# Performance work log

Hardware: AMD Instinct MI355X
Metric: run time of the kernel (lower is better)

## Reference

```python
import jax, jax.numpy as jnp
import numpy as np


def setup_inputs() -> dict:
    key = jax.random.key(0)
    k1, k2, k3, k4 = jax.random.split(key, 4)
    B, NITER, NSIZE, DIM = 4096, 8, 32, 64
    return {
        "self_vectors": jax.random.normal(k1, (B, NITER, DIM), dtype=jnp.float32),
        "neighbor_vectors": jax.random.normal(k2, (B, NITER * NSIZE, DIM), dtype=jnp.float32),
        "neighbor_relations": jax.random.normal(k3, (B, NITER * NSIZE, DIM), dtype=jnp.float32),
        "user_embeddings": jax.random.normal(k4, (B, DIM), dtype=jnp.float32),
        "neighbor_size": NSIZE,
    }


def reference(self_vectors, neighbor_vectors, neighbor_relations, user_embeddings, neighbor_size):
    B, neighbor_iter, dim = self_vectors.shape
    # reshape flat neighbor axis -> (B, neighbor_iter, neighbor_size, dim)
    nv = neighbor_vectors.reshape(B, neighbor_iter, neighbor_size, dim)
    nr = neighbor_relations.reshape(B, neighbor_iter, neighbor_size, dim)
    ue = user_embeddings.reshape(B, 1, 1, dim)
    # user-relation attention score per neighbor: mean over dim
    scores = jnp.mean(ue * nr, axis=-1)                       # [B, niter, nsize]
    weights = jax.nn.softmax(scores, axis=-1)[..., None]      # [B, niter, nsize, 1]
    # softmax-weighted neighbors, then mean over neighbor axis
    neighbors_aggregated = jnp.mean(weights * nv, axis=2)     # [B, niter, dim]
    return jax.nn.relu(neighbors_aggregated)
```

## Files before the change

### kernel.cpp

```cpp
#include <hip/hip_runtime.h>


constexpr int DIM = 64;
constexpr int NSIZE = 32;

__global__ __launch_bounds__(256) void Aggregator_kernel(
    const float* __restrict__ nv,
    const float* __restrict__ nr,
    const float* __restrict__ ue,
    float* __restrict__ out,
    int niter, int ntasks) {
  int wave = (int)((blockIdx.x * blockDim.x + threadIdx.x) >> 6);
  if (wave >= ntasks) return;
  int lane = (int)(threadIdx.x & 63);
  int b = wave / niter;

  const float* nr_base = nr + (size_t)wave * (NSIZE * DIM);
  const float* nv_base = nv + (size_t)wave * (NSIZE * DIM);
  const float* ue_base = ue + (size_t)b * DIM;

  int h = lane >> 5;
  int s = lane & 31;

  const float4* nr4 = (const float4*)(nr_base + s * DIM + h * 32);
  const float4* ue4 = (const float4*)(ue_base + h * 32);
  float p = 0.f;
#pragma unroll
  for (int j = 0; j < 8; ++j) {
    float4 a = nr4[j];
    float4 u = ue4[j];
    p = fmaf(a.x, u.x, p);
    p = fmaf(a.y, u.y, p);
    p = fmaf(a.z, u.z, p);
    p = fmaf(a.w, u.w, p);
  }
  p += __shfl_xor(p, 32);
  float sc = p * (1.0f / DIM);

  float m = sc;
#pragma unroll
  for (int k = 1; k < 32; k <<= 1) m = fmaxf(m, __shfl_xor(m, k));
  float e = __expf(sc - m);
  float sum = e;
#pragma unroll
  for (int k = 1; k < 32; k <<= 1) sum += __shfl_xor(sum, k);
  float w = e / (sum * (float)NSIZE);

  float acc = 0.f;
#pragma unroll
  for (int si = 0; si < NSIZE; ++si) {
    float ws = __int_as_float(__builtin_amdgcn_readlane(__float_as_int(w), si));
    acc = fmaf(ws, nv_base[si * DIM + lane], acc);
  }
  out[(size_t)wave * DIM + lane] = fmaxf(acc, 0.f);
}

extern "C" void kernel_launch(void* const* d_in, const int* in_sizes, int n_in,
                              void* d_out, int out_size, void* d_ws, size_t ws_size,
                              hipStream_t stream) {
  const float* nv = (const float*)d_in[1];
  const float* nr = (const float*)d_in[2];
  const float* ue = (const float*)d_in[3];
  float* out = (float*)d_out;

  int ntasks = in_sizes[0] / DIM;
  int niter  = in_sizes[0] / in_sizes[3];
  int blocks = (ntasks + 3) / 4;
  Aggregator_kernel<<<blocks, 256, 0, stream>>>(nv, nr, ue, out, niter, ntasks);
}
```

Measured before the change: 513.5 us.

## Remap lanes for fully coalesced float4 loads and issue all loads upfront

Each wave now loads its neighbor relations and neighbor vectors as contiguous float4 chunks. Lane q=lane&15 covers a 4-wide slice of dim, and each lane handles 8 neighbors. All 16 float4 loads are issued before any compute, to raise memory-level parallelism and cut the strided and scalar load patterns of the old code. The dot products, softmax and weighted sum are rebuilt around this layout using 16-lane shuffle reductions and cross-group shuffles. This costs more registers and extra shuffles, and only 16 lanes write the output as float4.

After: 514.4 us. Within noise of the previous version (+0.2%).

```diff
diff --git a/kernel.cpp b/kernel.cpp
--- a/kernel.cpp
+++ b/kernel.cpp
@@ -14,45 +14,68 @@
   if (wave >= ntasks) return;
   int lane = (int)(threadIdx.x & 63);
   int b = wave / niter;
+  int q = lane & 15;
 
-  const float* nr_base = nr + (size_t)wave * (NSIZE * DIM);
-  const float* nv_base = nv + (size_t)wave * (NSIZE * DIM);
-  const float* ue_base = ue + (size_t)b * DIM;
+  const float4* nr4 = (const float4*)(nr + (size_t)wave * (NSIZE * DIM));
+  const float4* nv4 = (const float4*)(nv + (size_t)wave * (NSIZE * DIM));
 
-  int h = lane >> 5;
-  int s = lane & 31;
+  float4 a[8], v[8];
+#pragma unroll
+  for (int j = 0; j < 8; ++j) a[j] = nr4[j * 64 + lane];
+  float4 u = ((const float4*)(ue + (size_t)b * DIM))[q];
+#pragma unroll
+  for (int j = 0; j < 8; ++j) v[j] = nv4[j * 64 + lane];
 
-  const float4* nr4 = (const float4*)(nr_base + s * DIM + h * 32);
-  const float4* ue4 = (const float4*)(ue_base + h * 32);
-  float p = 0.f;
+  float sc[8];
 #pragma unroll
   for (int j = 0; j < 8; ++j) {
-    float4 a = nr4[j];
-    float4 u = ue4[j];
-    p = fmaf(a.x, u.x, p);
-    p = fmaf(a.y, u.y, p);
-    p = fmaf(a.z, u.z, p);
-    p = fmaf(a.w, u.w, p);
+    float p = a[j].x * u.x;
+    p = fmaf(a[j].y, u.y, p);
+    p = fmaf(a[j].z, u.z, p);
+    p = fmaf(a[j].w, u.w, p);
+#pragma unroll
+    for (int k = 1; k < 16; k <<= 1) p += __shfl_xor(p, k);
+    sc[j] = p * (1.0f / DIM);
   }
-  p += __shfl_xor(p, 32);
-  float sc = p * (1.0f / DIM);
 
-  float m = sc;
+  float m = sc[0];
 #pragma unroll
-  for (int k = 1; k < 32; k <<= 1) m = fmaxf(m, __shfl_xor(m, k));
-  float e = __expf(sc - m);
-  float sum = e;
+  for (int j = 1; j < 8; ++j) m = fmaxf(m, sc[j]);
+  m = fmaxf(m, __shfl_xor(m, 16));
+  m = fmaxf(m, __shfl_xor(m, 32));
+  float e[8];
+  float z = 0.f;
 #pragma unroll
-  for (int k = 1; k < 32; k <<= 1) sum += __shfl_xor(sum, k);
-  float w = e / (sum * (float)NSIZE);
+  for (int j = 0; j < 8; ++j) {
+    e[j] = __expf(sc[j] - m);
+    z += e[j];
+  }
+  z += __shfl_xor(z, 16);
+  z += __shfl_xor(z, 32);
+  float inv = 1.0f / (z * (float)NSIZE);
 
-  float acc = 0.f;
+  float4 acc = make_float4(0.f, 0.f, 0.f, 0.f);
 #pragma unroll
-  for (int si = 0; si < NSIZE; ++si) {
-    float ws = __int_as_float(__builtin_amdgcn_readlane(__float_as_int(w), si));
-    acc = fmaf(ws, nv_base[si * DIM + lane], acc);
+  for (int j = 0; j < 8; ++j) {
+    float w = e[j] * inv;
+    acc.x = fmaf(w, v[j].x, acc.x);
+    acc.y = fmaf(w, v[j].y, acc.y);
+    acc.z = fmaf(w, v[j].z, acc.z);
+    acc.w = fmaf(w, v[j].w, acc.w);
   }
-  out[(size_t)wave * DIM + lane] = fmaxf(acc, 0.f);
+#pragma unroll
+  for (int k = 16; k < 64; k <<= 1) {
+    acc.x += __shfl_xor(acc.x, k);
+    acc.y += __shfl_xor(acc.y, k);
+    acc.z += __shfl_xor(acc.z, k);
+    acc.w += __shfl_xor(acc.w, k);
+  }
+
+  if (lane < 16) {
+    float4 r = make_float4(fmaxf(acc.x, 0.f), fmaxf(acc.y, 0.f),
+                           fmaxf(acc.z, 0.f), fmaxf(acc.w, 0.f));
+    ((float4*)(out + (size_t)wave * DIM))[q] = r;
+  }
 }
 
 extern "C" void kernel_launch(void* const* d_in, const int* in_sizes, int n_in,
```
